# Optimization experiments

Hardware: AMD Instinct MI355X
Metric: run time of the kernel (lower is better)

The kernel has to match this reference:

```python
import jax, jax.numpy as jnp
import numpy as np

B = 8192
D = 32
K = 8
H0 = 256
H1 = 256
PER = 3 * K + 1  # 25 params per dim
SCALE = 10.0
RMIN, RMAX = -SCALE / 2.0, SCALE / 2.0
MIN_BW = 1e-3; MIN_BH = 1e-3; MIN_KS = 1e-3
CUR_STEPS = 10000.0; CUR_START = 0.0
DX_MB = 1e-4   # distrax min_bin_size default
DX_MS = 1e-4   # distrax min_knot_slope default
DX_OFF = float(np.log(np.expm1(1.0 - DX_MS)))  # so softplus(0+off)+ms == 1


def _masks():
    deg_in = np.arange(1, D + 1)
    hd0 = np.arange(H0) % (D - 1) + 1
    hd1 = np.arange(H1) % (D - 1) + 1
    m0 = (hd0[:, None] >= deg_in[None, :]).astype(np.float32).T      # (D, H0)
    m1 = (hd1[:, None] >= hd0[None, :]).astype(np.float32).T        # (H0, H1)
    out_mask = (deg_in[:, None] > hd1[None, :]).astype(np.float32)  # (D, H1)
    per_mask = np.repeat(out_mask, PER, axis=0)                      # (D*PER, H1)
    return jnp.asarray(m0), jnp.asarray(m1), jnp.asarray(per_mask)

M0, M1, PER_MASK = _masks()


def made(y, W0, b0, W1, b1, W_out, b_out):
    h = jax.nn.gelu(y @ (W0 * M0) + b0)
    h = jax.nn.gelu(h @ (W1 * M1) + b1)
    proj = h @ (W_out.T * PER_MASK.T) + b_out  # (B, D*PER)
    return proj.reshape(y.shape[0], D, PER)


def _g(a, idx):
    return jnp.take_along_axis(a, idx[..., None], axis=-1)[..., 0]


def _knots(p, training_step):
    # module-level processing (rqs_from_params) ...
    w_raw, h_raw, s_raw = p[..., :K], p[..., K:2 * K], p[..., 2 * K:]
    lw = jax.nn.softmax(w_raw, axis=-1) * SCALE * (1.0 - K * MIN_BW) + MIN_BW
    lh = jax.nn.softmax(h_raw, axis=-1) * SCALE * (1.0 - K * MIN_BH) + MIN_BH
    ls = jax.nn.softplus(s_raw) + MIN_KS
    alpha = jnp.clip((jnp.asarray(training_step, jnp.float32) - CUR_START) / CUR_STEPS, 0.0, 1.0)
    bw = (1.0 - alpha) * (SCALE / K) + alpha * lw
    bh = (1.0 - alpha) * (SCALE / K) + alpha * lh
    sl = (1.0 - alpha) * 1.0 + alpha * ls
    bw = bw / jnp.sum(bw, axis=-1, keepdims=True) * SCALE
    bh = bh / jnp.sum(bh, axis=-1, keepdims=True) * SCALE
    # ... followed by distrax.RationalQuadraticSpline internal normalization
    widths = jax.nn.softmax(bw, axis=-1) * (SCALE - K * DX_MB) + DX_MB
    heights = jax.nn.softmax(bh, axis=-1) * (SCALE - K * DX_MB) + DX_MB
    slopes = jax.nn.softplus(sl + DX_OFF) + DX_MS  # (..., K+1)
    zpad = jnp.zeros_like(widths[..., :1])
    xp = RMIN + jnp.concatenate([zpad, jnp.cumsum(widths, axis=-1)], axis=-1)
    yp = RMIN + jnp.concatenate([zpad, jnp.cumsum(heights, axis=-1)], axis=-1)
    return xp, yp, widths, heights, slopes


def spline_fwd(p, x, training_step):
    xp, yp, w, h, d = _knots(p, training_step)
    inr = (x >= RMIN) & (x <= RMAX)
    xc = jnp.clip(x, RMIN, RMAX)
    idx = jnp.clip(jnp.sum((xc[..., None] >= xp[..., :-1]), axis=-1) - 1, 0, K - 1)
    xk, yk = _g(xp, idx), _g(yp, idx)
    wk, hk = _g(w, idx), _g(h, idx)
    dk, dk1 = _g(d, idx), _g(d, idx + 1)
    s = hk / wk
    xi = (xc - xk) / wk
    z1 = xi * (1.0 - xi)
    den = s + (dk1 + dk - 2.0 * s) * z1
    y = yk + hk * (s * xi * xi + dk * z1) / den
    ld = 2.0 * jnp.log(s) + jnp.log(dk1 * xi * xi + 2.0 * s * z1 + dk * (1.0 - xi) ** 2) - 2.0 * jnp.log(den)
    return jnp.where(inr, y, x), jnp.where(inr, ld, 0.0)


def spline_inv(p, y, training_step):
    xp, yp, w, h, d = _knots(p, training_step)
    inr = (y >= RMIN) & (y <= RMAX)
    yc = jnp.clip(y, RMIN, RMAX)
    idx = jnp.clip(jnp.sum((yc[..., None] >= yp[..., :-1]), axis=-1) - 1, 0, K - 1)
    xk, yk = _g(xp, idx), _g(yp, idx)
    wk, hk = _g(w, idx), _g(h, idx)
    dk, dk1 = _g(d, idx), _g(d, idx + 1)
    s = hk / wk
    t = yc - yk
    coef = dk1 + dk - 2.0 * s
    a = hk * (s - dk) + t * coef
    b = hk * dk - t * coef
    c = -s * t
    xi = 2.0 * c / (-b - jnp.sqrt(b * b - 4.0 * a * c))
    x = xi * wk + xk
    z1 = xi * (1.0 - xi)
    den = s + coef * z1
    ld = -(2.0 * jnp.log(s) + jnp.log(dk1 * xi * xi + 2.0 * s * z1 + dk * (1.0 - xi) ** 2) - 2.0 * jnp.log(den))
    return jnp.where(inr, x, y), jnp.where(inr, ld, 0.0)


def setup_inputs() -> dict:
    ks = jax.random.split(jax.random.key(0), 4)
    sd = lambda k, shp, fan: jax.random.normal(k, shp, jnp.float32) / np.sqrt(fan).astype(np.float32)
    return {
        "x": jax.random.normal(ks[0], (B, D), jnp.float32) * 1.5,
        "W0": sd(ks[1], (D, H0), D),
        "b0": jnp.zeros((H0,), jnp.float32),
        "W1": sd(ks[2], (H0, H1), H0),
        "b1": jnp.zeros((H1,), jnp.float32),
        "W_out": sd(ks[3], (D * PER, H1), H1),
        "b_out": jnp.zeros((D * PER,), jnp.float32),
        "forward": 0,
        "training_step": 10000,
    }


def reference(x, W0, b0, W1, b1, W_out, b_out, forward, training_step):
    if forward:
        p = made(x, W0, b0, W1, b1, W_out, b_out)  # (B, D, PER)
        z, ld = spline_fwd(p, x, training_step)
        return z, jnp.sum(ld, axis=1)
    z = x

    def body(carry, i):
        x_so, ldj = carry
        p = made(x_so, W0, b0, W1, b1, W_out, b_out)
        p_i = jax.lax.dynamic_index_in_dim(p, i, axis=1, keepdims=False)  # (B, PER)
        z_i = jax.lax.dynamic_index_in_dim(z, i, axis=1, keepdims=False)  # (B,)
        x_i, ld = spline_inv(p_i, z_i, training_step)
        return (x_so.at[:, i].set(x_i), ldj + ld), None

    init = (jnp.zeros_like(z), jnp.zeros((z.shape[0],), z.dtype))
    (x_fin, ldj), _ = jax.lax.scan(body, init, jnp.arange(D))
    return x_fin, ldj
```

## Files before the change

kernel.cpp:

```cpp
#include <hip/hip_runtime.h>

typedef _Float16 f16x8 __attribute__((ext_vector_type(8)));
typedef float f32x4 __attribute__((ext_vector_type(4)));

#define NB 8192
#define DD 32
#define PER 25
#define STRH 272

#define FENCE_C() do { asm volatile("" ::: "memory"); \
                       __builtin_amdgcn_sched_barrier(0); } while (0)
#define FENCE_HW() do { asm volatile("s_waitcnt lgkmcnt(0)" ::: "memory"); \
                        __builtin_amdgcn_sched_barrier(0); } while (0)

__device__ __forceinline__ float rcp_f(float x) { return __builtin_amdgcn_rcpf(x); }
__device__ __forceinline__ float gelu_f(float x) {
    float a = -1.5957691216057308f * (x + 0.044715f * x * x * x);
    return x * rcp_f(1.0f + __expf(a));
}
__device__ __forceinline__ float softplus_f(float x) {
    return (x > 20.0f) ? x : __logf(1.0f + __expf(x));
}
__device__ __forceinline__ int cntf(int d) {
    return (d <= 0) ? 0 : ((d <= 8) ? 9 * d : 72 + 8 * (d - 8));
}
__device__ __forceinline__ int porig(int u) {
    int d = (u < 72) ? (u / 9 + 1) : ((u - 72) / 8 + 9);
    int s = (u < 72) ? (u % 9) : ((u - 72) % 8);
    return s * 31 + (d - 1);
}

__global__ void prep_kernel(const float* __restrict__ W0, const float* __restrict__ b0,
                            const float* __restrict__ W1, const float* __restrict__ b1,
                            const float* __restrict__ Wout, const float* __restrict__ bout,
                            _Float16* __restrict__ W0F, _Float16* __restrict__ W1F,
                            _Float16* __restrict__ WoutF,
                            float* __restrict__ b0F, float* __restrict__ b1F,
                            float* __restrict__ boutF)
{
    const int total = 16384 + 131072 + 262144 + 512 + 512 + 1024;
    for (int e = blockIdx.x * blockDim.x + threadIdx.x; e < total;
         e += gridDim.x * blockDim.x) {
        if (e < 16384) {
            int i = e >> 9, r = e & 511, lane = r >> 3, j = r & 7;
            int c = lane & 15, k = ((lane >> 4) << 3) + j;
            int nn = cntf(i) - cntf(i - 1);
            float v = 0.0f;
            if (c < nn && k < i) v = W0[k * 256 + (c * 31 + i - 1)];
            W0F[e] = (_Float16)v;
        } else if (e < 16384 + 131072) {
            int m = e - 16384;
            int i = m >> 12, r = m & 4095, kt = r >> 9, r2 = r & 511;
            int lane = r2 >> 3, j = r2 & 7;
            int c = lane & 15, kpos = kt * 32 + ((lane >> 4) << 3) + j;
            int nn = cntf(i) - cntf(i - 1), chi = cntf(i);
            float v = 0.0f;
            if (c < nn && kpos < chi) v = W1[porig(kpos) * 256 + (c * 31 + i - 1)];
            W1F[m] = (_Float16)v;
        } else if (e < 16384 + 131072 + 262144) {
            int m = e - (16384 + 131072);
            int i = m >> 13, r = m & 8191, ct = r >> 12, r2 = r & 4095;
            int kt = r2 >> 9, r3 = r2 & 511, lane = r3 >> 3, j = r3 & 7;
            int par = ct * 16 + (lane & 15), kpos = kt * 32 + ((lane >> 4) << 3) + j;
            int chi = cntf(i);
            float v = 0.0f;
            if (par < 25 && kpos < chi) v = Wout[(i * 25 + par) * 256 + porig(kpos)];
            WoutF[m] = (_Float16)v;
        } else if (e < 409600 + 512) {
            int m = e - 409600;
            int i = m >> 4, c = m & 15;
            int nn = cntf(i) - cntf(i - 1);
            b0F[m] = (c < nn) ? b0[c * 31 + i - 1] : 0.0f;
        } else if (e < 410112 + 512) {
            int m = e - 410112;
            int i = m >> 4, c = m & 15;
            int nn = cntf(i) - cntf(i - 1);
            b1F[m] = (c < nn) ? b1[c * 31 + i - 1] : 0.0f;
        } else {
            int m = e - 410624;
            int i = m >> 5, c = m & 31;
            boutF[m] = (c < 25) ? bout[i * 25 + c] : 0.0f;
        }
    }
}

__global__ __launch_bounds__(64, 1) void inv_kernel(
    const float* __restrict__ z,
    const _Float16* __restrict__ W0F, const _Float16* __restrict__ W1F,
    const _Float16* __restrict__ WoutF,
    const float* __restrict__ b0F, const float* __restrict__ b1F,
    const float* __restrict__ boutF,
    const int* __restrict__ tstep_p,
    float* __restrict__ xout, float* __restrict__ ldj)
{
    __shared__ float zs[16 * 33];
    __shared__ float xs[16 * 33];
    __shared__ float ps[16 * 33];
    __shared__ __align__(16) _Float16 h0L[16 * STRH];
    __shared__ __align__(16) _Float16 h1L[16 * STRH];

    const int l = threadIdx.x;
    const int c16 = l & 15;
    const int g = l >> 4;
    const int row0 = blockIdx.x * 16;

    for (int idx = l; idx < 512; idx += 64) {
        int r = idx >> 5, c = idx & 31;
        zs[r * 33 + c] = z[row0 * 32 + idx];
    }
    {
        unsigned int* p0 = (unsigned int*)h0L;
        unsigned int* p1 = (unsigned int*)h1L;
        for (int idx = l; idx < 16 * STRH / 2; idx += 64) { p0[idx] = 0u; p1[idx] = 0u; }
    }

    f16x8 xfrag;
#pragma unroll
    for (int j = 0; j < 8; ++j) xfrag[j] = (_Float16)0.0f;

    const float alpha = fminf(fmaxf(((float)(*tstep_p)) / 10000.0f, 0.0f), 1.0f);
    const float oma = 1.0f - alpha;
    const float dxoff = logf(expm1f(0.9999f));

    float ldreg = 0.0f;

    f16x8 wa2[2];
    float b0v2[2], b1v2[2], boA2[2], boB2[2];
    wa2[0] = *(const f16x8*)&W0F[l * 8];
    b0v2[0] = b0F[c16];
    b1v2[0] = b1F[c16];
    boA2[0] = boutF[c16];
    boB2[0] = boutF[16 + c16];

    FENCE_HW();

#pragma unroll 1
    for (int ib = 0; ib < DD; ib += 2) {
#pragma unroll
        for (int ph = 0; ph < 2; ++ph) {
            const int i = ib + ph;
            const int clo = cntf(i - 1);
            const int chi = cntf(i);
            const int nn = chi - clo;
            const int ip = (i + 1 < DD) ? (i + 1) : (DD - 1);

            wa2[ph ^ 1] = *(const f16x8*)&W0F[ip * 512 + l * 8];
            b0v2[ph ^ 1] = b0F[ip * 16 + c16];
            b1v2[ph ^ 1] = b1F[ip * 16 + c16];
            boA2[ph ^ 1] = boutF[ip * 32 + c16];
            boB2[ph ^ 1] = boutF[ip * 32 + 16 + c16];

            f16x8 wb_r[8], wc_r[2][8];
#pragma unroll
            for (int kt = 0; kt < 8; ++kt)
                wb_r[kt] = *(const f16x8*)&W1F[i * 4096 + kt * 512 + l * 8];
#pragma unroll
            for (int ct = 0; ct < 2; ++ct)
#pragma unroll
                for (int kt = 0; kt < 8; ++kt)
                    wc_r[ct][kt] = *(const f16x8*)&WoutF[i * 8192 + ct * 4096 + kt * 512 + l * 8];

            if (nn > 0) {
                f32x4 acc;
#pragma unroll
                for (int q = 0; q < 4; ++q) acc[q] = 0.0f;
                acc = __builtin_amdgcn_mfma_f32_16x16x32_f16(xfrag, wa2[ph], acc, 0, 0, 0);
                float bb = b0v2[ph];
                if (c16 < nn) {
                    const int col = clo + c16;
#pragma unroll
                    for (int q = 0; q < 4; ++q) {
                        int row = g * 4 + q;
                        int phys = (col & ~31) | ((col & 31) ^ (8 * (row & 3)));
                        h0L[row * STRH + phys] = (_Float16)gelu_f(acc[q] + bb);
                    }
                }
            }
            FENCE_HW();

            if (nn > 0) {
                const int fbase = c16 * STRH + ((g ^ (c16 & 3)) << 3);
                f32x4 acc;
#pragma unroll
                for (int q = 0; q < 4; ++q) acc[q] = 0.0f;
#pragma unroll
                for (int kt = 0; kt < 8; ++kt) {
                    if (kt * 32 < chi) {
                        f16x8 af = *(const f16x8*)&h0L[fbase + kt * 32];
                        acc = __builtin_amdgcn_mfma_f32_16x16x32_f16(af, wb_r[kt], acc, 0, 0, 0);
                    }
                }
                float bb = b1v2[ph];
                if (c16 < nn) {
                    const int col = clo + c16;
#pragma unroll
                    for (int q = 0; q < 4; ++q) {
                        int row = g * 4 + q;
                        int phys = (col & ~31) | ((col & 31) ^ (8 * (row & 3)));
                        h1L[row * STRH + phys] = (_Float16)gelu_f(acc[q] + bb);
                    }
                }
            }
            FENCE_HW();

            {
                const int fbase = c16 * STRH + ((g ^ (c16 & 3)) << 3);
                f32x4 acc0, acc1;
#pragma unroll
                for (int q = 0; q < 4; ++q) { acc0[q] = 0.0f; acc1[q] = 0.0f; }
#pragma unroll
                for (int kt = 0; kt < 8; ++kt) {
                    if (kt * 32 < chi) {
                        f16x8 af = *(const f16x8*)&h1L[fbase + kt * 32];
                        acc0 = __builtin_amdgcn_mfma_f32_16x16x32_f16(af, wc_r[0][kt], acc0, 0, 0, 0);
                        acc1 = __builtin_amdgcn_mfma_f32_16x16x32_f16(af, wc_r[1][kt], acc1, 0, 0, 0);
                    }
                }
                float boA = boA2[ph], boB = boB2[ph];
#pragma unroll
                for (int q = 0; q < 4; ++q)
                    ps[(g * 4 + q) * 33 + c16] = acc0[q] + boA;
                if (16 + c16 < 25) {
#pragma unroll
                    for (int q = 0; q < 4; ++q)
                        ps[(g * 4 + q) * 33 + 16 + c16] = acc1[q] + boB;
                }
            }
            FENCE_HW();

            float xv_sel;
            {
                const int r4 = l >> 2;
                const int p  = l & 3;
                const int qb = l & ~3;

                const float* bp = &ps[r4 * 33];
                float w_a = bp[p],      w_b = bp[4 + p];
                float h_a = bp[8 + p],  h_b = bp[12 + p];
                float d_a = bp[16 + p], d_b = bp[20 + p], d_cin = bp[24];
                const float zi = zs[r4 * 33 + i];

                auto qsum = [](float v) {
                    v += __shfl_xor(v, 1); v += __shfl_xor(v, 2); return v;
                };
                auto qmax = [](float v) {
                    v = fmaxf(v, __shfl_xor(v, 1)); v = fmaxf(v, __shfl_xor(v, 2)); return v;
                };

                float m_w = qmax(fmaxf(w_a, w_b));
                float ewa = __expf(w_a - m_w), ewb = __expf(w_b - m_w);
                float rsw = rcp_f(qsum(ewa + ewb));
                float bwa = oma * 1.25f + alpha * (ewa * rsw * 9.92f + 0.001f);
                float bwb = oma * 1.25f + alpha * (ewb * rsw * 9.92f + 0.001f);
                float scw = 10.0f * rcp_f(qsum(bwa + bwb));
                bwa *= scw; bwb *= scw;
                float m2w = qmax(fmaxf(bwa, bwb));
                float e2wa = __expf(bwa - m2w), e2wb = __expf(bwb - m2w);
                float rs2w = rcp_f(qsum(e2wa + e2wb));
                float wdt_a = e2wa * rs2w * 9.9992f + 1e-4f;
                float wdt_b = e2wb * rs2w * 9.9992f + 1e-4f;

                float m_h = qmax(fmaxf(h_a, h_b));
                float eha = __expf(h_a - m_h), ehb = __expf(h_b - m_h);
                float rsh = rcp_f(qsum(eha + ehb));
                float bha = oma * 1.25f + alpha * (eha * rsh * 9.92f + 0.001f);
                float bhb = oma * 1.25f + alpha * (ehb * rsh * 9.92f + 0.001f);
                float sch = 10.0f * rcp_f(qsum(bha + bhb));
                bha *= sch; bhb *= sch;
                float m2h = qmax(fmaxf(bha, bhb));
                float e2ha = __expf(bha - m2h), e2hb = __expf(bhb - m2h);
                float rs2h = rcp_f(qsum(e2ha + e2hb));
                float hgt_a = e2ha * rs2h * 9.9992f + 1e-4f;
                float hgt_b = e2hb * rs2h * 9.9992f + 1e-4f;

                float dsl_a = softplus_f(oma + alpha * (softplus_f(d_a) + 0.001f) + dxoff) + 1e-4f;
                float dsl_b = softplus_f(oma + alpha * (softplus_f(d_b) + 0.001f) + dxoff) + 1e-4f;
                float dsl_c = softplus_f(oma + alpha * (softplus_f(d_cin) + 0.001f) + dxoff) + 1e-4f;

                float ca = wdt_a, tf;
                tf = __shfl_up(ca, 1); if (p >= 1) ca += tf;
                tf = __shfl_up(ca, 2); if (p >= 2) ca += tf;
                float cb = wdt_b;
                tf = __shfl_up(cb, 1); if (p >= 1) cb += tf;
                tf = __shfl_up(cb, 2); if (p >= 2) cb += tf;
                cb += __shfl(ca, qb + 3);

                float cha = hgt_a;
                tf = __shfl_up(cha, 1); if (p >= 1) cha += tf;
                tf = __shfl_up(cha, 2); if (p >= 2) cha += tf;
                float chb = hgt_b;
                tf = __shfl_up(chb, 1); if (p >= 1) chb += tf;
                tf = __shfl_up(chb, 2); if (p >= 2) chb += tf;
                chb += __shfl(cha, qb + 3);

                const bool inr = (zi >= -5.0f) && (zi <= 5.0f);
                const float yc = fminf(fmaxf(zi, -5.0f), 5.0f);

                unsigned long long B1 = __ballot(yc >= cha - 5.0f);
                unsigned long long B2 = __ballot((p < 3) && (yc >= chb - 5.0f));
                unsigned long long qm = 0xFull << qb;
                int idx = __popcll(B1 & qm) + __popcll(B2 & qm);

                int s0 = qb + (idx & 3);
                float wk = (idx < 4) ? __shfl(wdt_a, s0) : __shfl(wdt_b, s0);
                float hk = (idx < 4) ? __shfl(hgt_a, s0) : __shfl(hgt_b, s0);
                int im1 = idx - 1;
                int s1 = qb + (im1 & 3);
                float cwm = (im1 < 4) ? __shfl(ca, s1) : __shfl(cb, s1);
                float chm = (im1 < 4) ? __shfl(cha, s1) : __shfl(chb, s1);
                float xk = (idx == 0) ? -5.0f : (cwm - 5.0f);
                float yk = (idx == 0) ? -5.0f : (chm - 5.0f);
                float dk = (idx < 4) ? __shfl(dsl_a, s0) : __shfl(dsl_b, s0);
                int j1 = idx + 1;
                int s2l = qb + (j1 & 3);
                float d1a = __shfl(dsl_a, s2l), d1b = __shfl(dsl_b, s2l);
                float dk1 = (j1 < 4) ? d1a : ((j1 < 8) ? d1b : dsl_c);

                float s_ = hk * rcp_f(wk);
                float tt = yc - yk;
                float coef = dk1 + dk - 2.0f * s_;
                float aa = hk * (s_ - dk) + tt * coef;
                float bb = hk * dk - tt * coef;
                float cc = -s_ * tt;
                float disc = bb * bb - 4.0f * aa * cc;
                float xi = 2.0f * cc * rcp_f(-bb - __builtin_amdgcn_sqrtf(disc));
                float xv = xi * wk + xk;
                float z1 = xi * (1.0f - xi);
                float den = s_ + coef * z1;
                float omxi = 1.0f - xi;
                float ld = -(2.0f * __logf(s_) +
                             __logf(dk1 * xi * xi + 2.0f * s_ * z1 + dk * omxi * omxi)
                             - 2.0f * __logf(den));

                xv_sel = inr ? xv : zi;
                ldreg += inr ? ld : 0.0f;
                if (p == 0) xs[r4 * 33 + i] = xv_sel;
            }

            {
                float xnew = __shfl(xv_sel, (l & 15) << 2);
                if (g == (i >> 3)) {
#pragma unroll
                    for (int j = 0; j < 8; ++j)
                        if (j == (i & 7)) xfrag[j] = (_Float16)xnew;
                }
            }
            FENCE_C();
        }
    }

    FENCE_HW();
    for (int idx = l; idx < 512; idx += 64) {
        int r = idx >> 5, c = idx & 31;
        xout[row0 * 32 + idx] = xs[r * 33 + c];
    }
    if ((l & 3) == 0) ldj[row0 + (l >> 2)] = ldreg;
}

extern "C" void kernel_launch(void* const* d_in, const int* in_sizes, int n_in,
                              void* d_out, int out_size, void* d_ws, size_t ws_size,
                              hipStream_t stream)
{
    const float* z    = (const float*)d_in[0];
    const float* W0   = (const float*)d_in[1];
    const float* b0   = (const float*)d_in[2];
    const float* W1   = (const float*)d_in[3];
    const float* b1   = (const float*)d_in[4];
    const float* Wout = (const float*)d_in[5];
    const float* bout = (const float*)d_in[6];
    const int* tstep  = (const int*)d_in[8];

    float* out  = (float*)d_out;
    float* xout = out;
    float* ldj  = out + NB * DD;

    _Float16* W0F   = (_Float16*)d_ws;
    _Float16* W1F   = W0F + 16384;
    _Float16* WoutF = W1F + 131072;
    float* b0F  = (float*)(WoutF + 262144);
    float* b1F  = b0F + 512;
    float* boutF = b1F + 512;

    prep_kernel<<<1608, 256, 0, stream>>>(W0, b0, W1, b1, Wout, bout,
                                          W0F, W1F, WoutF, b0F, b1F, boutF);
    inv_kernel<<<NB / 16, 64, 0, stream>>>(z, W0F, W1F, WoutF, b0F, b1F, boutF,
                                           tstep, xout, ldj);
}
```

Before: 101.2 us.

## Prefetch next-step weights and split MFMA chains into safe and dependent parts

```diff
diff --git a/kernel.cpp b/kernel.cpp
--- a/kernel.cpp
+++ b/kernel.cpp
@@ -121,16 +121,26 @@
     const float alpha = fminf(fmaxf(((float)(*tstep_p)) / 10000.0f, 0.0f), 1.0f);
     const float oma = 1.0f - alpha;
     const float dxoff = logf(expm1f(0.9999f));
+    const int fbase = c16 * STRH + ((g ^ (c16 & 3)) << 3);
 
     float ldreg = 0.0f;
 
     f16x8 wa2[2];
     float b0v2[2], b1v2[2], boA2[2], boB2[2];
+    f16x8 wb_r[8], wc_r[2][8];
     wa2[0] = *(const f16x8*)&W0F[l * 8];
     b0v2[0] = b0F[c16];
     b1v2[0] = b1F[c16];
     boA2[0] = boutF[c16];
     boB2[0] = boutF[16 + c16];
+#pragma unroll
+    for (int kt = 0; kt < 8; ++kt)
+        wb_r[kt] = *(const f16x8*)&W1F[kt * 512 + l * 8];
+#pragma unroll
+    for (int ct = 0; ct < 2; ++ct)
+#pragma unroll
+        for (int kt = 0; kt < 8; ++kt)
+            wc_r[ct][kt] = *(const f16x8*)&WoutF[ct * 4096 + kt * 512 + l * 8];
 
     FENCE_HW();
 
@@ -143,89 +153,112 @@
             const int chi = cntf(i);
             const int nn = chi - clo;
             const int ip = (i + 1 < DD) ? (i + 1) : (DD - 1);
+            const int safeN = clo >> 5;
+
+            f16x8 af0[8], af1[8];
+#pragma unroll
+            for (int kt = 0; kt < 8; ++kt) {
+                if (kt < safeN) {
+                    af0[kt] = *(const f16x8*)&h0L[fbase + kt * 32];
+                    af1[kt] = *(const f16x8*)&h1L[fbase + kt * 32];
+                }
+            }
+            FENCE_C();
+
+            if (nn > 0) {
+                f32x4 acc;
+#pragma unroll
+                for (int q = 0; q < 4; ++q) acc[q] = 0.0f;
+                acc = __builtin_amdgcn_mfma_f32_16x16x32_f16(xfrag, wa2[ph], acc, 0, 0, 0);
+                float bb = b0v2[ph];
+                if (c16 < nn) {
+                    const int col = clo + c16;
+#pragma unroll
+                    for (int q = 0; q < 4; ++q) {
+                        int row = g * 4 + q;
+                        int phys = (col & ~31) | ((col & 31) ^ (8 * (row & 3)));
+                        h0L[row * STRH + phys] = (_Float16)gelu_f(acc[q] + bb);
+                    }
+                }
+            }
+            FENCE_C();
+
+            f32x4 accBE, accBO, accC0, accC1;
+#pragma unroll
+            for (int q = 0; q < 4; ++q) { accBE[q] = 0.0f; accBO[q] = 0.0f;
+                                          accC0[q] = 0.0f; accC1[q] = 0.0f; }
+#pragma unroll
+            for (int kt = 0; kt < 8; ++kt) {
+                if (kt < safeN) {
+                    if (kt & 1)
+                        accBO = __builtin_amdgcn_mfma_f32_16x16x32_f16(af0[kt], wb_r[kt], accBO, 0, 0, 0);
+                    else
+                        accBE = __builtin_amdgcn_mfma_f32_16x16x32_f16(af0[kt], wb_r[kt], accBE, 0, 0, 0);
+                    accC0 = __builtin_amdgcn_mfma_f32_16x16x32_f16(af1[kt], wc_r[0][kt], accC0, 0, 0, 0);
+                    accC1 = __builtin_amdgcn_mfma_f32_16x16x32_f16(af1[kt], wc_r[1][kt], accC1, 0, 0, 0);
+                }
+            }
+            FENCE_HW();
+
+            if (nn > 0) {
+#pragma unroll
+                for (int kt = 0; kt < 8; ++kt) {
+                    if (kt >= safeN && kt * 32 < chi) {
+                        f16x8 af = *(const f16x8*)&h0L[fbase + kt * 32];
+                        if (kt & 1)
+                            accBO = __builtin_amdgcn_mfma_f32_16x16x32_f16(af, wb_r[kt], accBO, 0, 0, 0);
+                        else
+                            accBE = __builtin_amdgcn_mfma_f32_16x16x32_f16(af, wb_r[kt], accBE, 0, 0, 0);
+                    }
+                }
+                float bb = b1v2[ph];
+                if (c16 < nn) {
+                    const int col = clo + c16;
+#pragma unroll
+                    for (int q = 0; q < 4; ++q) {
+                        int row = g * 4 + q;
+                        int phys = (col & ~31) | ((col & 31) ^ (8 * (row & 3)));
+                        h1L[row * STRH + phys] =
+                            (_Float16)gelu_f(accBE[q] + accBO[q] + bb);
+                    }
+                }
+            }
+            FENCE_HW();
+
+            {
+#pragma unroll
+                for (int kt = 0; kt < 8; ++kt) {
+                    if (kt >= safeN && kt * 32 < chi) {
+                        f16x8 af = *(const f16x8*)&h1L[fbase + kt * 32];
+                        accC0 = __builtin_amdgcn_mfma_f32_16x16x32_f16(af, wc_r[0][kt], accC0, 0, 0, 0);
+                        accC1 = __builtin_amdgcn_mfma_f32_16x16x32_f16(af, wc_r[1][kt], accC1, 0, 0, 0);
+                    }
+                }
+                float boA = boA2[ph], boB = boB2[ph];
+#pragma unroll
+                for (int q = 0; q < 4; ++q)
+                    ps[(g * 4 + q) * 33 + c16] = accC0[q] + boA;
+                if (16 + c16 < 25) {
+#pragma unroll
+                    for (int q = 0; q < 4; ++q)
+                        ps[(g * 4 + q) * 33 + 16 + c16] = accC1[q] + boB;
+                }
+            }
 
             wa2[ph ^ 1] = *(const f16x8*)&W0F[ip * 512 + l * 8];
             b0v2[ph ^ 1] = b0F[ip * 16 + c16];
             b1v2[ph ^ 1] = b1F[ip * 16 + c16];
             boA2[ph ^ 1] = boutF[ip * 32 + c16];
             boB2[ph ^ 1] = boutF[ip * 32 + 16 + c16];
-
-            f16x8 wb_r[8], wc_r[2][8];
 #pragma unroll
             for (int kt = 0; kt < 8; ++kt)
-                wb_r[kt] = *(const f16x8*)&W1F[i * 4096 + kt * 512 + l * 8];
+                wb_r[kt] = *(const f16x8*)&W1F[ip * 4096 + kt * 512 + l * 8];
 #pragma unroll
             for (int ct = 0; ct < 2; ++ct)
 #pragma unroll
                 for (int kt = 0; kt < 8; ++kt)
-                    wc_r[ct][kt] = *(const f16x8*)&WoutF[i * 8192 + ct * 4096 + kt * 512 + l * 8];
-
-            if (nn > 0) {
-                f32x4 acc;
-#pragma unroll
-                for (int q = 0; q < 4; ++q) acc[q] = 0.0f;
-                acc = __builtin_amdgcn_mfma_f32_16x16x32_f16(xfrag, wa2[ph], acc, 0, 0, 0);
-                float bb = b0v2[ph];
-                if (c16 < nn) {
-                    const int col = clo + c16;
-#pragma unroll
-                    for (int q = 0; q < 4; ++q) {
-                        int row = g * 4 + q;
-                        int phys = (col & ~31) | ((col & 31) ^ (8 * (row & 3)));
-                        h0L[row * STRH + phys] = (_Float16)gelu_f(acc[q] + bb);
-                    }
-                }
-            }
-            FENCE_HW();
-
-            if (nn > 0) {
-                const int fbase = c16 * STRH + ((g ^ (c16 & 3)) << 3);
-                f32x4 acc;
-#pragma unroll
-                for (int q = 0; q < 4; ++q) acc[q] = 0.0f;
-#pragma unroll
-                for (int kt = 0; kt < 8; ++kt) {
-                    if (kt * 32 < chi) {
-                        f16x8 af = *(const f16x8*)&h0L[fbase + kt * 32];
-                        acc = __builtin_amdgcn_mfma_f32_16x16x32_f16(af, wb_r[kt], acc, 0, 0, 0);
-                    }
-                }
-                float bb = b1v2[ph];
-                if (c16 < nn) {
-                    const int col = clo + c16;
-#pragma unroll
-                    for (int q = 0; q < 4; ++q) {
-                        int row = g * 4 + q;
-                        int phys = (col & ~31) | ((col & 31) ^ (8 * (row & 3)));
-                        h1L[row * STRH + phys] = (_Float16)gelu_f(acc[q] + bb);
-                    }
-                }
-            }
-            FENCE_HW();
-
-            {
-                const int fbase = c16 * STRH + ((g ^ (c16 & 3)) << 3);
-                f32x4 acc0, acc1;
-#pragma unroll
-                for (int q = 0; q < 4; ++q) { acc0[q] = 0.0f; acc1[q] = 0.0f; }
-#pragma unroll
-                for (int kt = 0; kt < 8; ++kt) {
-                    if (kt * 32 < chi) {
-                        f16x8 af = *(const f16x8*)&h1L[fbase + kt * 32];
-                        acc0 = __builtin_amdgcn_mfma_f32_16x16x32_f16(af, wc_r[0][kt], acc0, 0, 0, 0);
-                        acc1 = __builtin_amdgcn_mfma_f32_16x16x32_f16(af, wc_r[1][kt], acc1, 0, 0, 0);
-                    }
-                }
-                float boA = boA2[ph], boB = boB2[ph];
-#pragma unroll
-                for (int q = 0; q < 4; ++q)
-                    ps[(g * 4 + q) * 33 + c16] = acc0[q] + boA;
-                if (16 + c16 < 25) {
-#pragma unroll
-                    for (int q = 0; q < 4; ++q)
-                        ps[(g * 4 + q) * 33 + 16 + c16] = acc1[q] + boB;
-                }
-            }
+                    wc_r[ct][kt] = *(const f16x8*)&WoutF[ip * 8192 + ct * 4096 + kt * 512 + l * 8];
+
             FENCE_HW();
 
             float xv_sel;
@@ -328,9 +361,8 @@
                 float z1 = xi * (1.0f - xi);
                 float den = s_ + coef * z1;
                 float omxi = 1.0f - xi;
-                float ld = -(2.0f * __logf(s_) +
-                             __logf(dk1 * xi * xi + 2.0f * s_ * z1 + dk * omxi * omxi)
-                             - 2.0f * __logf(den));
+                float num = dk1 * xi * xi + 2.0f * s_ * z1 + dk * omxi * omxi;
+                float ld = __logf(den * den * rcp_f(s_ * s_ * num));
 
                 xv_sel = inr ? xv : zi;
                 ldreg += inr ? ld : 0.0f;
```

After: 106.7 us. 5.5% more time.

## Process two 16-row tiles per wave to share weight loads and interleave chains

Applied to the files above, without the earlier changes.

```diff
diff --git a/kernel.cpp b/kernel.cpp
--- a/kernel.cpp
+++ b/kernel.cpp
@@ -84,6 +84,112 @@
     }
 }
 
+__device__ __forceinline__ float spline_quad(const float* __restrict__ bp, float zi,
+                                             float alpha, float oma, float dxoff,
+                                             int l, float& ldacc)
+{
+    const int p  = l & 3;
+    const int qb = l & ~3;
+
+    float w_a = bp[p],      w_b = bp[4 + p];
+    float h_a = bp[8 + p],  h_b = bp[12 + p];
+    float d_a = bp[16 + p], d_b = bp[20 + p], d_cin = bp[24];
+
+    auto qsum = [](float v) {
+        v += __shfl_xor(v, 1); v += __shfl_xor(v, 2); return v;
+    };
+    auto qmax = [](float v) {
+        v = fmaxf(v, __shfl_xor(v, 1)); v = fmaxf(v, __shfl_xor(v, 2)); return v;
+    };
+
+    float m_w = qmax(fmaxf(w_a, w_b));
+    float ewa = __expf(w_a - m_w), ewb = __expf(w_b - m_w);
+    float rsw = rcp_f(qsum(ewa + ewb));
+    float bwa = oma * 1.25f + alpha * (ewa * rsw * 9.92f + 0.001f);
+    float bwb = oma * 1.25f + alpha * (ewb * rsw * 9.92f + 0.001f);
+    float scw = 10.0f * rcp_f(qsum(bwa + bwb));
+    bwa *= scw; bwb *= scw;
+    float m2w = qmax(fmaxf(bwa, bwb));
+    float e2wa = __expf(bwa - m2w), e2wb = __expf(bwb - m2w);
+    float rs2w = rcp_f(qsum(e2wa + e2wb));
+    float wdt_a = e2wa * rs2w * 9.9992f + 1e-4f;
+    float wdt_b = e2wb * rs2w * 9.9992f + 1e-4f;
+
+    float m_h = qmax(fmaxf(h_a, h_b));
+    float eha = __expf(h_a - m_h), ehb = __expf(h_b - m_h);
+    float rsh = rcp_f(qsum(eha + ehb));
+    float bha = oma * 1.25f + alpha * (eha * rsh * 9.92f + 0.001f);
+    float bhb = oma * 1.25f + alpha * (ehb * rsh * 9.92f + 0.001f);
+    float sch = 10.0f * rcp_f(qsum(bha + bhb));
+    bha *= sch; bhb *= sch;
+    float m2h = qmax(fmaxf(bha, bhb));
+    float e2ha = __expf(bha - m2h), e2hb = __expf(bhb - m2h);
+    float rs2h = rcp_f(qsum(e2ha + e2hb));
+    float hgt_a = e2ha * rs2h * 9.9992f + 1e-4f;
+    float hgt_b = e2hb * rs2h * 9.9992f + 1e-4f;
+
+    float dsl_a = softplus_f(oma + alpha * (softplus_f(d_a) + 0.001f) + dxoff) + 1e-4f;
+    float dsl_b = softplus_f(oma + alpha * (softplus_f(d_b) + 0.001f) + dxoff) + 1e-4f;
+    float dsl_c = softplus_f(oma + alpha * (softplus_f(d_cin) + 0.001f) + dxoff) + 1e-4f;
+
+    float ca = wdt_a, tf;
+    tf = __shfl_up(ca, 1); if (p >= 1) ca += tf;
+    tf = __shfl_up(ca, 2); if (p >= 2) ca += tf;
+    float cb = wdt_b;
+    tf = __shfl_up(cb, 1); if (p >= 1) cb += tf;
+    tf = __shfl_up(cb, 2); if (p >= 2) cb += tf;
+    cb += __shfl(ca, qb + 3);
+
+    float cha = hgt_a;
+    tf = __shfl_up(cha, 1); if (p >= 1) cha += tf;
+    tf = __shfl_up(cha, 2); if (p >= 2) cha += tf;
+    float chb = hgt_b;
+    tf = __shfl_up(chb, 1); if (p >= 1) chb += tf;
+    tf = __shfl_up(chb, 2); if (p >= 2) chb += tf;
+    chb += __shfl(cha, qb + 3);
+
+    const bool inr = (zi >= -5.0f) && (zi <= 5.0f);
+    const float yc = fminf(fmaxf(zi, -5.0f), 5.0f);
+
+    unsigned long long B1 = __ballot(yc >= cha - 5.0f);
+    unsigned long long B2 = __ballot((p < 3) && (yc >= chb - 5.0f));
+    unsigned long long qm = 0xFull << qb;
+    int idx = __popcll(B1 & qm) + __popcll(B2 & qm);
+
+    int s0 = qb + (idx & 3);
+    float wk = (idx < 4) ? __shfl(wdt_a, s0) : __shfl(wdt_b, s0);
+    float hk = (idx < 4) ? __shfl(hgt_a, s0) : __shfl(hgt_b, s0);
+    int im1 = idx - 1;
+    int s1 = qb + (im1 & 3);
+    float cwm = (im1 < 4) ? __shfl(ca, s1) : __shfl(cb, s1);
+    float chm = (im1 < 4) ? __shfl(cha, s1) : __shfl(chb, s1);
+    float xk = (idx == 0) ? -5.0f : (cwm - 5.0f);
+    float yk = (idx == 0) ? -5.0f : (chm - 5.0f);
+    float dk = (idx < 4) ? __shfl(dsl_a, s0) : __shfl(dsl_b, s0);
+    int j1 = idx + 1;
+    int s2l = qb + (j1 & 3);
+    float d1a = __shfl(dsl_a, s2l), d1b = __shfl(dsl_b, s2l);
+    float dk1 = (j1 < 4) ? d1a : ((j1 < 8) ? d1b : dsl_c);
+
+    float s_ = hk * rcp_f(wk);
+    float tt = yc - yk;
+    float coef = dk1 + dk - 2.0f * s_;
+    float aa = hk * (s_ - dk) + tt * coef;
+    float bb = hk * dk - tt * coef;
+    float cc = -s_ * tt;
+    float disc = bb * bb - 4.0f * aa * cc;
+    float xi = 2.0f * cc * rcp_f(-bb - __builtin_amdgcn_sqrtf(disc));
+    float xv = xi * wk + xk;
+    float z1 = xi * (1.0f - xi);
+    float den = s_ + coef * z1;
+    float omxi = 1.0f - xi;
+    float num = dk1 * xi * xi + 2.0f * s_ * z1 + dk * omxi * omxi;
+    float ld = __logf(den * den * rcp_f(s_ * s_ * num));
+
+    ldacc += inr ? ld : 0.0f;
+    return inr ? xv : zi;
+}
+
 __global__ __launch_bounds__(64, 1) void inv_kernel(
     const float* __restrict__ z,
     const _Float16* __restrict__ W0F, const _Float16* __restrict__ W1F,
@@ -93,36 +199,38 @@
     const int* __restrict__ tstep_p,
     float* __restrict__ xout, float* __restrict__ ldj)
 {
-    __shared__ float zs[16 * 33];
-    __shared__ float xs[16 * 33];
-    __shared__ float ps[16 * 33];
-    __shared__ __align__(16) _Float16 h0L[16 * STRH];
-    __shared__ __align__(16) _Float16 h1L[16 * STRH];
+    __shared__ float zs[2][16 * 33];
+    __shared__ float xs[2][16 * 33];
+    __shared__ float ps[2][16 * 33];
+    __shared__ __align__(16) _Float16 h0L[2][16 * STRH];
+    __shared__ __align__(16) _Float16 h1L[2][16 * STRH];
 
     const int l = threadIdx.x;
     const int c16 = l & 15;
     const int g = l >> 4;
-    const int row0 = blockIdx.x * 16;
-
-    for (int idx = l; idx < 512; idx += 64) {
-        int r = idx >> 5, c = idx & 31;
-        zs[r * 33 + c] = z[row0 * 32 + idx];
+    const int row0 = blockIdx.x * 32;
+
+    for (int idx = l; idx < 1024; idx += 64) {
+        int t = idx >> 9, rem = idx & 511;
+        int r = rem >> 5, c = rem & 31;
+        zs[t][r * 33 + c] = z[row0 * 32 + idx];
     }
     {
         unsigned int* p0 = (unsigned int*)h0L;
         unsigned int* p1 = (unsigned int*)h1L;
-        for (int idx = l; idx < 16 * STRH / 2; idx += 64) { p0[idx] = 0u; p1[idx] = 0u; }
-    }
-
-    f16x8 xfrag;
-#pragma unroll
-    for (int j = 0; j < 8; ++j) xfrag[j] = (_Float16)0.0f;
+        for (int idx = l; idx < 2 * 16 * STRH / 2; idx += 64) { p0[idx] = 0u; p1[idx] = 0u; }
+    }
+
+    f16x8 xfrag0, xfrag1;
+#pragma unroll
+    for (int j = 0; j < 8; ++j) { xfrag0[j] = (_Float16)0.0f; xfrag1[j] = (_Float16)0.0f; }
 
     const float alpha = fminf(fmaxf(((float)(*tstep_p)) / 10000.0f, 0.0f), 1.0f);
     const float oma = 1.0f - alpha;
     const float dxoff = logf(expm1f(0.9999f));
-
-    float ldreg = 0.0f;
+    const int fbase = c16 * STRH + ((g ^ (c16 & 3)) << 3);
+
+    float ldreg0 = 0.0f, ldreg1 = 0.0f;
 
     f16x8 wa2[2];
     float b0v2[2], b1v2[2], boA2[2], boB2[2];
@@ -144,27 +252,28 @@
             const int nn = chi - clo;
             const int ip = (i + 1 < DD) ? (i + 1) : (DD - 1);
 
+            f16x8 wb_r[8], wc_r[2][8];
+#pragma unroll
+            for (int kt = 0; kt < 8; ++kt)
+                wb_r[kt] = *(const f16x8*)&W1F[i * 4096 + kt * 512 + l * 8];
+#pragma unroll
+            for (int ct = 0; ct < 2; ++ct)
+#pragma unroll
+                for (int kt = 0; kt < 8; ++kt)
+                    wc_r[ct][kt] = *(const f16x8*)&WoutF[i * 8192 + ct * 4096 + kt * 512 + l * 8];
+
             wa2[ph ^ 1] = *(const f16x8*)&W0F[ip * 512 + l * 8];
             b0v2[ph ^ 1] = b0F[ip * 16 + c16];
             b1v2[ph ^ 1] = b1F[ip * 16 + c16];
             boA2[ph ^ 1] = boutF[ip * 32 + c16];
             boB2[ph ^ 1] = boutF[ip * 32 + 16 + c16];
 
-            f16x8 wb_r[8], wc_r[2][8];
-#pragma unroll
-            for (int kt = 0; kt < 8; ++kt)
-                wb_r[kt] = *(const f16x8*)&W1F[i * 4096 + kt * 512 + l * 8];
-#pragma unroll
-            for (int ct = 0; ct < 2; ++ct)
-#pragma unroll
-                for (int kt = 0; kt < 8; ++kt)
-                    wc_r[ct][kt] = *(const f16x8*)&WoutF[i * 8192 + ct * 4096 + kt * 512 + l * 8];
-
             if (nn > 0) {
-                f32x4 acc;
-#pragma unroll
-                for (int q = 0; q < 4; ++q) acc[q] = 0.0f;
-                acc = __builtin_amdgcn_mfma_f32_16x16x32_f16(xfrag, wa2[ph], acc, 0, 0, 0);
+                f32x4 a0, a1;
+#pragma unroll
+                for (int q = 0; q < 4; ++q) { a0[q] = 0.0f; a1[q] = 0.0f; }
+                a0 = __builtin_amdgcn_mfma_f32_16x16x32_f16(xfrag0, wa2[ph], a0, 0, 0, 0);
+                a1 = __builtin_amdgcn_mfma_f32_16x16x32_f16(xfrag1, wa2[ph], a1, 0, 0, 0);
                 float bb = b0v2[ph];
                 if (c16 < nn) {
                     const int col = clo + c16;
@@ -172,22 +281,24 @@
                     for (int q = 0; q < 4; ++q) {
                         int row = g * 4 + q;
                         int phys = (col & ~31) | ((col & 31) ^ (8 * (row & 3)));
-                        h0L[row * STRH + phys] = (_Float16)gelu_f(acc[q] + bb);
+                        h0L[0][row * STRH + phys] = (_Float16)gelu_f(a0[q] + bb);
+                        h0L[1][row * STRH + phys] = (_Float16)gelu_f(a1[q] + bb);
                     }
                 }
             }
             FENCE_HW();
 
             if (nn > 0) {
-                const int fbase = c16 * STRH + ((g ^ (c16 & 3)) << 3);
-                f32x4 acc;
-#pragma unroll
-                for (int q = 0; q < 4; ++q) acc[q] = 0.0f;
+                f32x4 bA0, bA1;
+#pragma unroll
+                for (int q = 0; q < 4; ++q) { bA0[q] = 0.0f; bA1[q] = 0.0f; }
 #pragma unroll
                 for (int kt = 0; kt < 8; ++kt) {
                     if (kt * 32 < chi) {
-                        f16x8 af = *(const f16x8*)&h0L[fbase + kt * 32];
-                        acc = __builtin_amdgcn_mfma_f32_16x16x32_f16(af, wb_r[kt], acc, 0, 0, 0);
+                        f16x8 af0 = *(const f16x8*)&h0L[0][fbase + kt * 32];
+                        f16x8 af1 = *(const f16x8*)&h0L[1][fbase + kt * 32];
+                        bA0 = __builtin_amdgcn_mfma_f32_16x16x32_f16(af0, wb_r[kt], bA0, 0, 0, 0);
+                        bA1 = __builtin_amdgcn_mfma_f32_16x16x32_f16(af1, wb_r[kt], bA1, 0, 0, 0);
                     }
                 }
                 float bb = b1v2[ph];
@@ -197,152 +308,65 @@
                     for (int q = 0; q < 4; ++q) {
                         int row = g * 4 + q;
                         int phys = (col & ~31) | ((col & 31) ^ (8 * (row & 3)));
-                        h1L[row * STRH + phys] = (_Float16)gelu_f(acc[q] + bb);
+                        h1L[0][row * STRH + phys] = (_Float16)gelu_f(bA0[q] + bb);
+                        h1L[1][row * STRH + phys] = (_Float16)gelu_f(bA1[q] + bb);
                     }
                 }
             }
             FENCE_HW();
 
             {
-                const int fbase = c16 * STRH + ((g ^ (c16 & 3)) << 3);
-                f32x4 acc0, acc1;
-#pragma unroll
-                for (int q = 0; q < 4; ++q) { acc0[q] = 0.0f; acc1[q] = 0.0f; }
+                f32x4 c00, c01, c10, c11;
+#pragma unroll
+                for (int q = 0; q < 4; ++q) { c00[q] = 0.0f; c01[q] = 0.0f;
+                                              c10[q] = 0.0f; c11[q] = 0.0f; }
 #pragma unroll
                 for (int kt = 0; kt < 8; ++kt) {
                     if (kt * 32 < chi) {
-                        f16x8 af = *(const f16x8*)&h1L[fbase + kt * 32];
-                        acc0 = __builtin_amdgcn_mfma_f32_16x16x32_f16(af, wc_r[0][kt], acc0, 0, 0, 0);
-                        acc1 = __builtin_amdgcn_mfma_f32_16x16x32_f16(af, wc_r[1][kt], acc1, 0, 0, 0);
+                        f16x8 af0 = *(const f16x8*)&h1L[0][fbase + kt * 32];
+                        f16x8 af1 = *(const f16x8*)&h1L[1][fbase + kt * 32];
+                        c00 = __builtin_amdgcn_mfma_f32_16x16x32_f16(af0, wc_r[0][kt], c00, 0, 0, 0);
+                        c01 = __builtin_amdgcn_mfma_f32_16x16x32_f16(af0, wc_r[1][kt], c01, 0, 0, 0);
+                        c10 = __builtin_amdgcn_mfma_f32_16x16x32_f16(af1, wc_r[0][kt], c10, 0, 0, 0);
+                        c11 = __builtin_amdgcn_mfma_f32_16x16x32_f16(af1, wc_r[1][kt], c11, 0, 0, 0);
                     }
                 }
                 float boA = boA2[ph], boB = boB2[ph];
 #pragma unroll
-                for (int q = 0; q < 4; ++q)
-                    ps[(g * 4 + q) * 33 + c16] = acc0[q] + boA;
+                for (int q = 0; q < 4; ++q) {
+                    ps[0][(g * 4 + q) * 33 + c16] = c00[q] + boA;
+                    ps[1][(g * 4 + q) * 33 + c16] = c10[q] + boA;
+                }
                 if (16 + c16 < 25) {
 #pragma unroll
-                    for (int q = 0; q < 4; ++q)
-                        ps[(g * 4 + q) * 33 + 16 + c16] = acc1[q] + boB;
+                    for (int q = 0; q < 4; ++q) {
+                        ps[0][(g * 4 + q) * 33 + 16 + c16] = c01[q] + boB;
+                        ps[1][(g * 4 + q) * 33 + 16 + c16] = c11[q] + boB;
+                    }
                 }
             }
             FENCE_HW();
 
-            float xv_sel;
+            const int r4 = l >> 2;
+            float xv0 = spline_quad(&ps[0][r4 * 33], zs[0][r4 * 33 + i],
+                                    alpha, oma, dxoff, l, ldreg0);
+            float xv1 = spline_quad(&ps[1][r4 * 33], zs[1][r4 * 33 + i],
+                                    alpha, oma, dxoff, l, ldreg1);
+            if ((l & 3) == 0) {
+                xs[0][r4 * 33 + i] = xv0;
+                xs[1][r4 * 33 + i] = xv1;
+            }
+
             {
-                const int r4 = l >> 2;
-                const int p  = l & 3;
-                const int qb = l & ~3;
-
-                const float* bp = &ps[r4 * 33];
-                float w_a = bp[p],      w_b = bp[4 + p];
-                float h_a = bp[8 + p],  h_b = bp[12 + p];
-                float d_a = bp[16 + p], d_b = bp[20 + p], d_cin = bp[24];
-                const float zi = zs[r4 * 33 + i];
-
-                auto qsum = [](float v) {
-                    v += __shfl_xor(v, 1); v += __shfl_xor(v, 2); return v;
-                };
-                auto qmax = [](float v) {
-                    v = fmaxf(v, __shfl_xor(v, 1)); v = fmaxf(v, __shfl_xor(v, 2)); return v;
-                };
-
-                float m_w = qmax(fmaxf(w_a, w_b));
-                float ewa = __expf(w_a - m_w), ewb = __expf(w_b - m_w);
-                float rsw = rcp_f(qsum(ewa + ewb));
-                float bwa = oma * 1.25f + alpha * (ewa * rsw * 9.92f + 0.001f);
-                float bwb = oma * 1.25f + alpha * (ewb * rsw * 9.92f + 0.001f);
-                float scw = 10.0f * rcp_f(qsum(bwa + bwb));
-                bwa *= scw; bwb *= scw;
-                float m2w = qmax(fmaxf(bwa, bwb));
-                float e2wa = __expf(bwa - m2w), e2wb = __expf(bwb - m2w);
-                float rs2w = rcp_f(qsum(e2wa + e2wb));
-                float wdt_a = e2wa * rs2w * 9.9992f + 1e-4f;
-                float wdt_b = e2wb * rs2w * 9.9992f + 1e-4f;
-
-                float m_h = qmax(fmaxf(h_a, h_b));
-                float eha = __expf(h_a - m_h), ehb = __expf(h_b - m_h);
-                float rsh = rcp_f(qsum(eha + ehb));
-                float bha = oma * 1.25f + alpha * (eha * rsh * 9.92f + 0.001f);
-                float bhb = oma * 1.25f + alpha * (ehb * rsh * 9.92f + 0.001f);
-                float sch = 10.0f * rcp_f(qsum(bha + bhb));
-                bha *= sch; bhb *= sch;
-                float m2h = qmax(fmaxf(bha, bhb));
-                float e2ha = __expf(bha - m2h), e2hb = __expf(bhb - m2h);
-                float rs2h = rcp_f(qsum(e2ha + e2hb));
-                float hgt_a = e2ha * rs2h * 9.9992f + 1e-4f;
-                float hgt_b = e2hb * rs2h * 9.9992f + 1e-4f;
-
-                float dsl_a = softplus_f(oma + alpha * (softplus_f(d_a) + 0.001f) + dxoff) + 1e-4f;
-                float dsl_b = softplus_f(oma + alpha * (softplus_f(d_b) + 0.001f) + dxoff) + 1e-4f;
-                float dsl_c = softplus_f(oma + alpha * (softplus_f(d_cin) + 0.001f) + dxoff) + 1e-4f;
-
-                float ca = wdt_a, tf;
-                tf = __shfl_up(ca, 1); if (p >= 1) ca += tf;
-                tf = __shfl_up(ca, 2); if (p >= 2) ca += tf;
-                float cb = wdt_b;
-                tf = __shfl_up(cb, 1); if (p >= 1) cb += tf;
-                tf = __shfl_up(cb, 2); if (p >= 2) cb += tf;
-                cb += __shfl(ca, qb + 3);
-
-                float cha = hgt_a;
-                tf = __shfl_up(cha, 1); if (p >= 1) cha += tf;
-                tf = __shfl_up(cha, 2); if (p >= 2) cha += tf;
-                float chb = hgt_b;
-                tf = __shfl_up(chb, 1); if (p >= 1) chb += tf;
-                tf = __shfl_up(chb, 2); if (p >= 2) chb += tf;
-                chb += __shfl(cha, qb + 3);
-
-                const bool inr = (zi >= -5.0f) && (zi <= 5.0f);
-                const float yc = fminf(fmaxf(zi, -5.0f), 5.0f);
-
-                unsigned long long B1 = __ballot(yc >= cha - 5.0f);
-                unsigned long long B2 = __ballot((p < 3) && (yc >= chb - 5.0f));
-                unsigned long long qm = 0xFull << qb;
-                int idx = __popcll(B1 & qm) + __popcll(B2 & qm);
-
-                int s0 = qb + (idx & 3);
-                float wk = (idx < 4) ? __shfl(wdt_a, s0) : __shfl(wdt_b, s0);
-                float hk = (idx < 4) ? __shfl(hgt_a, s0) : __shfl(hgt_b, s0);
-                int im1 = idx - 1;
-                int s1 = qb + (im1 & 3);
-                float cwm = (im1 < 4) ? __shfl(ca, s1) : __shfl(cb, s1);
-                float chm = (im1 < 4) ? __shfl(cha, s1) : __shfl(chb, s1);
-                float xk = (idx == 0) ? -5.0f : (cwm - 5.0f);
-                float yk = (idx == 0) ? -5.0f : (chm - 5.0f);
-                float dk = (idx < 4) ? __shfl(dsl_a, s0) : __shfl(dsl_b, s0);
-                int j1 = idx + 1;
-                int s2l = qb + (j1 & 3);
-                float d1a = __shfl(dsl_a, s2l), d1b = __shfl(dsl_b, s2l);
-                float dk1 = (j1 < 4) ? d1a : ((j1 < 8) ? d1b : dsl_c);
-
-                float s_ = hk * rcp_f(wk);
-                float tt = yc - yk;
-                float coef = dk1 + dk - 2.0f * s_;
-                float aa = hk * (s_ - dk) + tt * coef;
-                float bb = hk * dk - tt * coef;
-                float cc = -s_ * tt;
-                float disc = bb * bb - 4.0f * aa * cc;
-                float xi = 2.0f * cc * rcp_f(-bb - __builtin_amdgcn_sqrtf(disc));
-                float xv = xi * wk + xk;
-                float z1 = xi * (1.0f - xi);
-                float den = s_ + coef * z1;
-                float omxi = 1.0f - xi;
-                float ld = -(2.0f * __logf(s_) +
-                             __logf(dk1 * xi * xi + 2.0f * s_ * z1 + dk * omxi * omxi)
-                             - 2.0f * __logf(den));
-
-                xv_sel = inr ? xv : zi;
-                ldreg += inr ? ld : 0.0f;
-                if (p == 0) xs[r4 * 33 + i] = xv_sel;
-            }
-
-            {
-                float xnew = __shfl(xv_sel, (l & 15) << 2);
+                float xn0 = __shfl(xv0, (l & 15) << 2);
+                float xn1 = __shfl(xv1, (l & 15) << 2);
                 if (g == (i >> 3)) {
 #pragma unroll
                     for (int j = 0; j < 8; ++j)
-                        if (j == (i & 7)) xfrag[j] = (_Float16)xnew;
+                        if (j == (i & 7)) {
+                            xfrag0[j] = (_Float16)xn0;
+                            xfrag1[j] = (_Float16)xn1;
+                        }
                 }
             }
             FENCE_C();
@@ -350,11 +374,16 @@
     }
 
     FENCE_HW();
-    for (int idx = l; idx < 512; idx += 64) {
-        int r = idx >> 5, c = idx & 31;
-        xout[row0 * 32 + idx] = xs[r * 33 + c];
-    }
-    if ((l & 3) == 0) ldj[row0 + (l >> 2)] = ldreg;
+    for (int idx = l; idx < 1024; idx += 64) {
+        int t = idx >> 9, rem = idx & 511;
+        int r = rem >> 5, c = rem & 31;
+        xout[row0 * 32 + idx] = xs[t][r * 33 + c];
+    }
+    if ((l & 3) == 0) {
+        int r4 = l >> 2;
+        ldj[row0 + r4] = ldreg0;
+        ldj[row0 + 16 + r4] = ldreg1;
+    }
 }
 
 extern "C" void kernel_launch(void* const* d_in, const int* in_sizes, int n_in,
@@ -383,6 +412,6 @@
 
     prep_kernel<<<1608, 256, 0, stream>>>(W0, b0, W1, b1, Wout, bout,
                                           W0F, W1F, WoutF, b0F, b1F, boutF);
-    inv_kernel<<<NB / 16, 64, 0, stream>>>(z, W0F, W1F, WoutF, b0F, b1F, boutF,
+    inv_kernel<<<NB / 32, 64, 0, stream>>>(z, W0F, W1F, WoutF, b0F, b1F, boutF,
                                            tstep, xout, ldj);
 }
```

New measurement: 153.3 us. 51.4% more time.
